# Performance work log

Hardware: AMD Instinct MI355X
Metric: run time of the kernel (lower is better)

Reference implementation:

```python
import jax, jax.numpy as jnp
import numpy as np

DIM = 512
NUM_HEADS = 8
EXPAND = 3
D1 = EXPAND * DIM          # 1536, divisible by NUM_HEADS
HEAD_DIM = D1 // NUM_HEADS  # 192
RPE_DIM = 64
RPE_LAYERS = 3
GLU_DIM = 1024
GAMMA = 0.999
EPS = 1e-8


def srms(x):
    # SimpleRMSNorm: x / (||x||_2 / sqrt(d) + eps), parameter-free
    d = x.shape[-1]
    rms = jnp.linalg.norm(x, axis=-1, keepdims=True) * (d ** -0.5)
    return x / (rms + EPS)


def setup_inputs() -> dict:
    key = jax.random.key(0)
    ks = jax.random.split(key, 12)
    def w(k, shape):
        return jax.random.normal(k, shape, dtype=jnp.float32) * 0.02
    B, H, W = 16, 32, 32
    return {
        "x": jax.random.normal(ks[0], (B, H * W, DIM), dtype=jnp.float32),
        "u_w": w(ks[1], (DIM, D1)), "u_b": jnp.zeros((D1,), jnp.float32),
        "v_w": w(ks[2], (DIM, D1)), "v_b": jnp.zeros((D1,), jnp.float32),
        "o_w": w(ks[3], (D1, DIM)), "o_b": jnp.zeros((DIM,), jnp.float32),
        "pos_w": w(ks[4], (2, RPE_DIM)), "pos_b": jnp.zeros((RPE_DIM,), jnp.float32),
        "rpe_lw": w(ks[5], (RPE_LAYERS, RPE_DIM, RPE_DIM)),
        "rpe_lb": jnp.zeros((RPE_LAYERS, RPE_DIM), jnp.float32),
        "rpe_ow": w(ks[6], (RPE_DIM, NUM_HEADS * HEAD_DIM)),
        "rpe_ob": jnp.zeros((NUM_HEADS * HEAD_DIM,), jnp.float32),
        "l1_w": w(ks[7], (DIM, GLU_DIM)), "l1_b": jnp.zeros((GLU_DIM,), jnp.float32),
        "l2_w": w(ks[8], (DIM, GLU_DIM)), "l2_b": jnp.zeros((GLU_DIM,), jnp.float32),
        "l3_w": w(ks[9], (GLU_DIM, DIM)), "l3_b": jnp.zeros((DIM,), jnp.float32),
        "H": H, "W": W,
    }


def _rpe(pos, pos_w, pos_b, rpe_lw, rpe_lb, rpe_ow, rpe_ob):
    # pos: (P, 2) relative 2D offsets -> (P, NUM_HEADS*HEAD_DIM) Toeplitz coefficients
    x = pos @ pos_w + pos_b
    for i in range(RPE_LAYERS):  # norm -> act -> linear
        x = jax.nn.silu(srms(x)) @ rpe_lw[i] + rpe_lb[i]
    return jax.nn.silu(srms(x)) @ rpe_ow + rpe_ob


def _gtu2d(x, H, W, u_w, u_b, v_w, v_b, o_w, o_b,
           pos_w, pos_b, rpe_lw, rpe_lb, rpe_ow, rpe_ob):
    B, N, _ = x.shape
    u = jax.nn.silu(x @ u_w + u_b)                 # (B, N, D1)
    v = jax.nn.silu(x @ v_w + v_b)                 # (B, N, D1)
    v = v.reshape(B, H, W, NUM_HEADS, HEAD_DIM).transpose(0, 3, 1, 2, 4)  # b h H W d
    # circular layout of relative offsets for FFT lengths (2H, 2W):
    # index a in [0, 2H) maps to offset a if a < H else a - 2H
    di = jnp.concatenate([jnp.arange(H), jnp.arange(-H, 0)]).astype(jnp.float32)
    dj = jnp.concatenate([jnp.arange(W), jnp.arange(-W, 0)]).astype(jnp.float32)
    pos = jnp.stack(jnp.meshgrid(di, dj, indexing="ij"), axis=-1)  # (2H, 2W, 2)
    coef = _rpe(pos.reshape(-1, 2), pos_w, pos_b, rpe_lw, rpe_lb, rpe_ow, rpe_ob)
    coef = coef.reshape(2 * H, 2 * W, NUM_HEADS, HEAD_DIM).transpose(2, 0, 1, 3)  # h 2H 2W d
    # decay mask gamma^(|di|+|dj|)
    decay = GAMMA ** (jnp.abs(di)[:, None] + jnp.abs(dj)[None, :])  # (2H, 2W)
    coef = coef * decay[None, :, :, None]
    # block-Toeplitz token mixing as 2D circular convolution via FFT
    vf = jnp.fft.rfft2(v, s=(2 * H, 2 * W), axes=(2, 3))
    cf = jnp.fft.rfft2(coef, s=(2 * H, 2 * W), axes=(1, 2))
    out = jnp.fft.irfft2(vf * cf[None], s=(2 * H, 2 * W), axes=(2, 3))[:, :, :H, :W, :]
    out = out.transpose(0, 2, 3, 1, 4).reshape(B, N, D1)
    return (u * out) @ o_w + o_b


def reference(x, u_w, u_b, v_w, v_b, o_w, o_b, pos_w, pos_b,
              rpe_lw, rpe_lb, rpe_ow, rpe_ob,
              l1_w, l1_b, l2_w, l2_b, l3_w, l3_b, H, W):
    x = x + _gtu2d(x, H, W, u_w, u_b, v_w, v_b, o_w, o_b,
                   pos_w, pos_b, rpe_lw, rpe_lb, rpe_ow, rpe_ob)
    mlp = (jax.nn.silu(x @ l1_w + l1_b) * (x @ l2_w + l2_b)) @ l3_w + l3_b
    return x + srms(mlp)
```

## Files before the change

kernel.cpp:

```cpp
#include <hip/hip_runtime.h>
#include <math.h>

#define B_   16
#define NN   1024
#define DIM_ 512
#define D1_  1536
#define GLU_ 1024

typedef unsigned short u16;
typedef __attribute__((ext_vector_type(8))) short bf16x8;
typedef __attribute__((ext_vector_type(4))) float f32x4;

__device__ __forceinline__ float silu_f(float x) {
    return x / (1.0f + __expf(-x));
}
__device__ __forceinline__ u16 f2b(float f) {
    unsigned u = __float_as_uint(f);
    return (u16)((u + 0x7FFF + ((u >> 16) & 1)) >> 16);
}
__device__ __forceinline__ float b2f(u16 s) {
    return __uint_as_float(((unsigned)s) << 16);
}

__launch_bounds__(256)
__global__ void prep_kernel(const float* __restrict__ x, u16* __restrict__ xb,
                            const float* __restrict__ u_w, u16* __restrict__ uwT,
                            const float* __restrict__ v_w, u16* __restrict__ vwT,
                            const float* __restrict__ o_w, u16* __restrict__ owT,
                            const float* __restrict__ l1_w, const float* __restrict__ l2_w,
                            u16* __restrict__ gluT,
                            const float* __restrict__ l3_w, u16* __restrict__ l3T,
                            const float* __restrict__ rpe_ow, u16* __restrict__ owT2,
                            const float* __restrict__ l1_b, const float* __restrict__ l2_b,
                            float* __restrict__ gluB,
                            const float* __restrict__ pos_w, const float* __restrict__ pos_b,
                            const float* __restrict__ lw, const float* __restrict__ lb,
                            u16* __restrict__ y) {
    __shared__ __align__(16) char smem_raw[4352];
    int bb = blockIdx.x;
    int t = threadIdx.x;
    if (bb < 2048) {
        #pragma unroll
        for (int j = 0; j < 4; ++j) {
            int i = bb * 1024 + j * 256 + t;
            float4 f = reinterpret_cast<const float4*>(x)[i];
            unsigned lo = (unsigned)f2b(f.x) | ((unsigned)f2b(f.y) << 16);
            unsigned hi = (unsigned)f2b(f.z) | ((unsigned)f2b(f.w) << 16);
            reinterpret_cast<uint2*>(xb)[i] = make_uint2(lo, hi);
        }
    } else if (bb < 5984) {
        const float* in; u16* out; int K, N, tile;
        if (bb < 2816)      { in = u_w;  out = uwT;  K = 512;  N = 1536; tile = bb - 2048; }
        else if (bb < 3584) { in = v_w;  out = vwT;  K = 512;  N = 1536; tile = bb - 2816; }
        else if (bb < 4352) { in = o_w;  out = owT;  K = 1536; N = 512;  tile = bb - 3584; }
        else if (bb < 4864) { in = l1_w; out = gluT; K = 512;  N = 1024; tile = bb - 4352; }
        else if (bb < 5376) { in = l2_w; out = gluT + (size_t)GLU_ * DIM_; K = 512; N = 1024; tile = bb - 4864; }
        else if (bb < 5888) { in = l3_w; out = l3T;  K = 1024; N = 512;  tile = bb - 5376; }
        else                { in = rpe_ow; out = owT2; K = 64; N = 1536; tile = bb - 5888; }
        float (*tl)[33] = (float(*)[33])smem_raw;
        int tiles_x = N >> 5;
        int n0 = (tile % tiles_x) * 32, k0 = (tile / tiles_x) * 32;
        int tx = t & 31, ty = t >> 5;
        #pragma unroll
        for (int r = 0; r < 32; r += 8)
            tl[ty + r][tx] = in[(size_t)(k0 + ty + r) * N + n0 + tx];
        __syncthreads();
        #pragma unroll
        for (int r = 0; r < 32; r += 8)
            out[(size_t)(n0 + ty + r) * K + k0 + tx] = f2b(tl[tx][ty + r]);
    } else if (bb < 5992) {
        int i = (bb - 5984) * 256 + t;
        gluB[i] = (i < 1024) ? l1_b[i] : l2_b[i - 1024];
    } else {
        float (*yb)[64] = (float(*)[64])smem_raw;
        int lane = t & 63;
        int wv = t >> 6;
        int a = (bb - 5992) * 4 + wv;
        int a1 = a >> 6, a2 = a & 63;
        float di = (a1 < 32) ? (float)a1 : (float)(a1 - 64);
        float dj = (a2 < 32) ? (float)a2 : (float)(a2 - 64);
        float xv = di * pos_w[lane] + dj * pos_w[64 + lane] + pos_b[lane];
        for (int L = 0; L < 3; ++L) {
            float ss = xv * xv;
            #pragma unroll
            for (int o = 32; o > 0; o >>= 1) ss += __shfl_xor(ss, o, 64);
            float yv = silu_f(xv / (sqrtf(ss) * 0.125f + 1e-8f));
            yb[wv][lane] = yv;
            __syncthreads();
            float acc = lb[L * 64 + lane];
            const float* w = lw + L * 4096 + lane;
            #pragma unroll 8
            for (int k = 0; k < 64; ++k) acc = fmaf(yb[wv][k], w[k * 64], acc);
            __syncthreads();
            xv = acc;
        }
        float ss = xv * xv;
        #pragma unroll
        for (int o = 32; o > 0; o >>= 1) ss += __shfl_xor(ss, o, 64);
        float yv = silu_f(xv / (sqrtf(ss) * 0.125f + 1e-8f));
        y[(size_t)a * 64 + lane] = f2b(yv);
    }
}

__global__ void coef_tt_kernel(const u16* __restrict__ coefD, u16* __restrict__ coefTT) {
    int t = threadIdx.x;
    int jg = blockIdx.x;
    int ct = blockIdx.y;
    int c  = ct * 64 + (t & 63);
    int jj = t >> 6;
    int dj = jg * 4 + jj;
    float adj = (dj < 32) ? (float)dj : (float)(64 - dj);
    #pragma unroll
    for (int oi = 0; oi < 8; ++oi) {
        u16 vals[8];
        #pragma unroll
        for (int m2 = 0; m2 < 8; ++m2) {
            int di = oi * 8 + m2;
            float adi = (di < 32) ? (float)di : (float)(64 - di);
            float decay = __expf(-0.0010005003335835344f * (adi + adj));
            vals[m2] = f2b(b2f(coefD[(size_t)(di * 64 + dj) * D1_ + c]) * decay);
        }
        *reinterpret_cast<uint4*>(&coefTT[(size_t)c * 4096 + dj * 64 + oi * 8]) =
            *reinterpret_cast<uint4*>(vals);
    }
}

template<int EPI, int PERMB>
__launch_bounds__(256, 4)
__global__ void mfma_gemm(const u16* __restrict__ A, const u16* __restrict__ BT,
                          const float* __restrict__ bias, const float* __restrict__ R,
                          void* __restrict__ C0, void* __restrict__ C1,
                          int M, int N, int K) {
    __shared__ __align__(16) u16 Asmem[128 * 64];
    __shared__ __align__(16) u16 Bsmem[128 * 64];
    int nwg = gridDim.x * gridDim.y;
    int bid = blockIdx.y * gridDim.x + blockIdx.x;
    int qq = nwg >> 3, rr = nwg & 7;
    int xcd = bid & 7, lid = bid >> 3;
    int swz = (xcd < rr ? xcd * (qq + 1) : rr * (qq + 1) + (xcd - rr) * qq) + lid;
    int bx = swz % gridDim.x, by = swz / gridDim.x;
    int tid = threadIdx.x;
    int w = tid >> 6, lane = tid & 63;
    int lr = lane & 15, kg = lane >> 4;
    int wr = w >> 1, wc = w & 1;
    int m0 = by * 128, n0 = bx * 128;
    f32x4 acc[4][4] = {};
    for (int k0 = 0; k0 < K; k0 += 64) {
        #pragma unroll
        for (int r = 0; r < 4; ++r) {
            int c4 = (r * 4 + w) * 64 + lane;
            int row = c4 >> 3, slot = c4 & 7;
            int sl = slot ^ (row & 7);
            const u16* ga = A + (size_t)(m0 + row) * K + k0 + sl * 8;
            int grow = n0 + row;
            if (PERMB == 1) {
                grow = (grow & ~1023) | ((grow & 31) << 5) | ((grow >> 5) & 31);
            } else if (PERMB == 2) {
                int c = grow & 127;
                int f = ((grow >> 7) << 6) + ((c >> 6) << 5) + (((c >> 5) & 1) << 4) + (c & 15);
                grow = (((c >> 4) & 1) << 10) + f;
            }
            const u16* gb = BT + (size_t)grow * K + k0 + sl * 8;
            u16* la = Asmem + (r * 4 + w) * 512;
            u16* lb = Bsmem + (r * 4 + w) * 512;
            __builtin_amdgcn_global_load_lds((const __attribute__((address_space(1))) void*)ga,
                                             (__attribute__((address_space(3))) void*)la, 16, 0, 0);
            __builtin_amdgcn_global_load_lds((const __attribute__((address_space(1))) void*)gb,
                                             (__attribute__((address_space(3))) void*)lb, 16, 0, 0);
        }
        __syncthreads();
        #pragma unroll
        for (int kk = 0; kk < 2; ++kk) {
            bf16x8 af[4], bfr[4];
            #pragma unroll
            for (int m = 0; m < 4; ++m) {
                int row = wr * 64 + m * 16 + lr;
                int sl = (kk * 4 + kg) ^ (row & 7);
                af[m] = *reinterpret_cast<const bf16x8*>(&Asmem[row * 64 + sl * 8]);
            }
            #pragma unroll
            for (int n = 0; n < 4; ++n) {
                int row = wc * 64 + n * 16 + lr;
                int sl = (kk * 4 + kg) ^ (row & 7);
                bfr[n] = *reinterpret_cast<const bf16x8*>(&Bsmem[row * 64 + sl * 8]);
            }
            #pragma unroll
            for (int m = 0; m < 4; ++m)
                #pragma unroll
                for (int n = 0; n < 4; ++n)
                    acc[m][n] = __builtin_amdgcn_mfma_f32_16x16x32_bf16(af[m], bfr[n], acc[m][n], 0, 0, 0);
        }
        __syncthreads();
    }
    if (EPI == 5) {
        #pragma unroll
        for (int m = 0; m < 4; ++m) {
            #pragma unroll
            for (int np = 0; np < 2; ++np) {
                int n = np * 2;
                int f = (n0 >> 1) + wc * 32 + np * 16 + lr;
                #pragma unroll
                for (int q = 0; q < 4; ++q) {
                    int row = m0 + wr * 64 + m * 16 + kg * 4 + q;
                    float a1 = acc[m][n][q] + bias[f];
                    float a2 = acc[m][n + 1][q] + bias[1024 + f];
                    ((u16*)C0)[(size_t)row * GLU_ + f] = f2b(silu_f(a1) * a2);
                }
            }
        }
    } else {
        #pragma unroll
        for (int m = 0; m < 4; ++m) {
            #pragma unroll
            for (int n = 0; n < 4; ++n) {
                #pragma unroll
                for (int q = 0; q < 4; ++q) {
                    int row = m0 + wr * 64 + m * 16 + kg * 4 + q;
                    int col = n0 + wc * 64 + n * 16 + lr;
                    size_t idx = (size_t)row * N + col;
                    if (EPI == 0) {
                        float vv = acc[m][n][q] + bias[col];
                        ((u16*)C0)[idx] = f2b(silu_f(vv));
                    } else if (EPI == 1) {
                        float t2 = acc[m][n][q] + bias[col] + R[idx];
                        ((float*)C0)[idx] = t2;
                        ((u16*)C1)[idx] = f2b(t2);
                    } else if (EPI == 2) {
                        ((u16*)C0)[idx] = f2b(acc[m][n][q] + bias[col]);
                    } else if (EPI == 3) {
                        ((float*)C0)[idx] = acc[m][n][q] + bias[col];
                    } else {
                        float vv = acc[m][n][q] + bias[row];
                        ((u16*)C0)[idx] = f2b(silu_f(vv));
                    }
                }
            }
        }
    }
}

__launch_bounds__(512, 1)
__global__ void conv_mfma_kernel(const u16* __restrict__ coefTT, const u16* __restrict__ vT2,
                                 u16* __restrict__ mixT) {
    __shared__ __align__(16) u16 vlds[16384];
    __shared__ __align__(16) u16 gt[32768];
    __shared__ __align__(16) u16 d2l[4096];
    int c = blockIdx.x;
    int t = threadIdx.x;
    int wv = t >> 6, lane = t & 63;
    int lr = lane & 15, kg = lane >> 4;
    int lrs = lr & 7;

    int mbc[4];
    #pragma unroll
    for (int nt = 0; nt < 4; ++nt)
        mbc[nt] = (((kg * 8 - (nt * 8 + wv)) & 63) & ~7) >> 3;

    #pragma unroll
    for (int pass = 0; pass < 4; ++pass) {
        int L = pass * 512 + t;
        int b = L >> 7, k8s = L & 127;
        int k8 = k8s ^ (b & 7);
        const u16* src = vT2 + (size_t)c * 16384 + b * 1024 + k8 * 8;
        u16* dst = vlds + (size_t)(pass * 512 + wv * 64) * 8;
        __builtin_amdgcn_global_load_lds((const __attribute__((address_space(1))) void*)src,
                                         (__attribute__((address_space(3))) void*)dst, 16, 0, 0);
    }
    {
        const u16* src = coefTT + (size_t)c * 4096 + t * 8;
        u16* dst = d2l + wv * 512;
        __builtin_amdgcn_global_load_lds((const __attribute__((address_space(1))) void*)src,
                                         (__attribute__((address_space(3))) void*)dst, 16, 0, 0);
    }
    __syncthreads();

    for (int e = t; e < 32768; e += 512) {
        int m = e & 63, w = (e >> 6) & 63, o = e >> 12;
        int oo = (8 - o) & 7;
        int q = (64 - ((m + oo) & 63)) & 63;
        gt[(o * 64 + w) * 64 + ((m >> 3) ^ (w & 7)) * 8 + (m & 7)] = d2l[w * 64 + q];
    }
    __syncthreads();

    f32x4 acc[4][2] = {};
    const bf16x8* vb8 = (const bf16x8*)vlds;
    const bf16x8* gtw = (const bf16x8*)gt + wv * 512;
    for (int jp = 0; jp < 32; ++jp) {
        bf16x8 af = vb8[lr * 128 + ((jp * 4 + kg) ^ lrs)];
        int w0 = (lr - jp) & 63;
        int w1 = (w0 + 16) & 63;
        #pragma unroll
        for (int nt = 0; nt < 4; ++nt) {
            bf16x8 b0 = gtw[w0 * 8 + (mbc[nt] ^ (w0 & 7))];
            acc[nt][0] = __builtin_amdgcn_mfma_f32_16x16x32_bf16(af, b0, acc[nt][0], 0, 0, 0);
            bf16x8 b1 = gtw[w1 * 8 + (mbc[nt] ^ (w1 & 7))];
            acc[nt][1] = __builtin_amdgcn_mfma_f32_16x16x32_bf16(af, b1, acc[nt][1], 0, 0, 0);
        }
    }
    __syncthreads();

    #pragma unroll
    for (int nt = 0; nt < 4; ++nt) {
        #pragma unroll
        for (int h = 0; h < 2; ++h) {
            int p = nt * 256 + wv * 32 + h * 16 + lr;
            #pragma unroll
            for (int q = 0; q < 4; ++q) {
                int b = kg * 4 + q;
                vlds[b * 1024 + (p ^ ((b & 7) << 3))] = f2b(acc[nt][h][q]);
            }
        }
    }
    __syncthreads();

    const uint4* src16 = (const uint4*)vlds;
    #pragma unroll
    for (int pass = 0; pass < 4; ++pass) {
        int L = pass * 512 + t;
        int b = L >> 7;
        int pc = (L & 127) ^ (b & 7);
        uint4 val = src16[L];
        *reinterpret_cast<uint4*>(mixT + (size_t)c * 16384 + b * 1024 + pc * 8) = val;
    }
}

__launch_bounds__(256)
__global__ void mult_kernel(const u16* __restrict__ mixT, u16* __restrict__ u) {
    int r = blockIdx.x * 256 + threadIdx.x;
    int c0 = blockIdx.y * 64;
    #pragma unroll
    for (int oc = 0; oc < 8; ++oc) {
        int cb = c0 + oc * 8;
        float mv[8];
        #pragma unroll
        for (int m2 = 0; m2 < 8; ++m2)
            mv[m2] = b2f(mixT[(size_t)(cb + m2) * 16384 + r]);
        u16 uv[8];
        *reinterpret_cast<uint4*>(uv) = *reinterpret_cast<const uint4*>(&u[(size_t)r * D1_ + cb]);
        #pragma unroll
        for (int m2 = 0; m2 < 8; ++m2) uv[m2] = f2b(b2f(uv[m2]) * mv[m2]);
        *reinterpret_cast<uint4*>(&u[(size_t)r * D1_ + cb]) = *reinterpret_cast<uint4*>(uv);
    }
}

__launch_bounds__(256)
__global__ void final_kernel(const float* __restrict__ x2, const float* __restrict__ m,
                             float* __restrict__ out) {
    int row = blockIdx.x;
    const float* mr = m + (size_t)row * DIM_;
    const float* xr = x2 + (size_t)row * DIM_;
    float* orow = out + (size_t)row * DIM_;
    int t = threadIdx.x;
    float a = mr[t], b2 = mr[t + 256];
    float ss = a * a + b2 * b2;
    #pragma unroll
    for (int o = 32; o > 0; o >>= 1) ss += __shfl_xor(ss, o, 64);
    __shared__ float red[4];
    int wid = t >> 6;
    if ((t & 63) == 0) red[wid] = ss;
    __syncthreads();
    float tot = red[0] + red[1] + red[2] + red[3];
    float inv = 1.0f / (sqrtf(tot) * 0.044194173824159216f + 1e-8f);
    orow[t]       = xr[t]       + a  * inv;
    orow[t + 256] = xr[t + 256] + b2 * inv;
}

extern "C" void kernel_launch(void* const* d_in, const int* in_sizes, int n_in,
                              void* d_out, int out_size, void* d_ws, size_t ws_size,
                              hipStream_t stream) {
    const float* x     = (const float*)d_in[0];
    const float* u_w   = (const float*)d_in[1];
    const float* u_b   = (const float*)d_in[2];
    const float* v_w   = (const float*)d_in[3];
    const float* v_b   = (const float*)d_in[4];
    const float* o_w   = (const float*)d_in[5];
    const float* o_b   = (const float*)d_in[6];
    const float* pos_w = (const float*)d_in[7];
    const float* pos_b = (const float*)d_in[8];
    const float* rpe_lw = (const float*)d_in[9];
    const float* rpe_lb = (const float*)d_in[10];
    const float* rpe_ow = (const float*)d_in[11];
    const float* rpe_ob = (const float*)d_in[12];
    const float* l1_w  = (const float*)d_in[13];
    const float* l1_b  = (const float*)d_in[14];
    const float* l2_w  = (const float*)d_in[15];
    const float* l2_b  = (const float*)d_in[16];
    const float* l3_w  = (const float*)d_in[17];
    const float* l3_b  = (const float*)d_in[18];
    float* out = (float*)d_out;

    u16* coefD  = (u16*)d_ws;
    u16* coefTT = coefD + 6291456;
    u16* xb     = coefTT + 6291456;
    u16* u      = xb + 8388608;
    u16* vT2    = u + 25165824;
    u16* mixT   = vT2 + 25165824;
    float* x2   = (float*)(mixT + 25165824);
    u16* x2b    = (u16*)(x2 + 8388608);
    u16* uwT    = x2b + 8388608;
    u16* vwT    = uwT + 786432;
    u16* owT    = vwT + 786432;
    u16* gluT   = owT + 786432;
    u16* l3T    = gluT + 1048576;
    float* gluB = (float*)(l3T + 524288);
    u16* y      = (u16*)(gluB + 2048);
    u16* owT2   = y + 262144;
    u16* p      = u;
    float* mm   = (float*)vT2;

    const int M = B_ * NN;

    prep_kernel<<<7016, 256, 0, stream>>>(x, xb, u_w, uwT, v_w, vwT, o_w, owT,
                                          l1_w, l2_w, gluT, l3_w, l3T, rpe_ow, owT2,
                                          l1_b, l2_b, gluB, pos_w, pos_b, rpe_lw, rpe_lb, y);
    mfma_gemm<2, 0><<<dim3(D1_ / 128, 4096 / 128), 256, 0, stream>>>(y, owT2, rpe_ob, nullptr, coefD, nullptr, 4096, D1_, 64);
    coef_tt_kernel<<<dim3(16, 24), 256, 0, stream>>>(coefD, coefTT);
    mfma_gemm<4, 1><<<dim3(M / 128, D1_ / 128), 256, 0, stream>>>(vwT, xb, v_b, nullptr, vT2, nullptr, D1_, M, DIM_);
    conv_mfma_kernel<<<1536, 512, 0, stream>>>(coefTT, vT2, mixT);
    mfma_gemm<0, 0><<<dim3(D1_ / 128, M / 128), 256, 0, stream>>>(xb, uwT, u_b, nullptr, u, nullptr, M, D1_, DIM_);
    mult_kernel<<<dim3(M / 256, D1_ / 64), 256, 0, stream>>>(mixT, u);
    mfma_gemm<1, 0><<<dim3(DIM_ / 128, M / 128), 256, 0, stream>>>(u, owT, o_b, x, x2, x2b, M, DIM_, D1_);
    mfma_gemm<5, 2><<<dim3(2 * GLU_ / 128, M / 128), 256, 0, stream>>>(x2b, gluT, gluB, nullptr, p, nullptr, M, 2 * GLU_, DIM_);
    mfma_gemm<3, 0><<<dim3(DIM_ / 128, M / 128), 256, 0, stream>>>(p, l3T, l3_b, nullptr, mm, nullptr, M, DIM_, GLU_);
    final_kernel<<<M, 256, 0, stream>>>(x2, mm, out);
}
```

Measured before the change: 396.4 us.

## Fuse decay transpose into coef GEMM epilogue and store residual/MLP in bf16

Removes the separate coef_tt_kernel by computing the coefficient GEMM transposed (weights as A, permuted positions as B) and applying the decay factor in a new epilogue, writing coefTT directly. It also drops the fp32 copies of the residual x2 and the l3 output, keeping only bf16 versions that final_kernel reads. This cuts a launch and a sizeable amount of fp32 memory traffic. The cost is precision: the residual stream added into the output is now rounded to bf16.

```diff
diff --git a/kernel.cpp b/kernel.cpp
--- a/kernel.cpp
+++ b/kernel.cpp
@@ -99,29 +99,6 @@
         for (int o = 32; o > 0; o >>= 1) ss += __shfl_xor(ss, o, 64);
         float yv = silu_f(xv / (sqrtf(ss) * 0.125f + 1e-8f));
         y[(size_t)a * 64 + lane] = f2b(yv);
-    }
-}
-
-__global__ void coef_tt_kernel(const u16* __restrict__ coefD, u16* __restrict__ coefTT) {
-    int t = threadIdx.x;
-    int jg = blockIdx.x;
-    int ct = blockIdx.y;
-    int c  = ct * 64 + (t & 63);
-    int jj = t >> 6;
-    int dj = jg * 4 + jj;
-    float adj = (dj < 32) ? (float)dj : (float)(64 - dj);
-    #pragma unroll
-    for (int oi = 0; oi < 8; ++oi) {
-        u16 vals[8];
-        #pragma unroll
-        for (int m2 = 0; m2 < 8; ++m2) {
-            int di = oi * 8 + m2;
-            float adi = (di < 32) ? (float)di : (float)(64 - di);
-            float decay = __expf(-0.0010005003335835344f * (adi + adj));
-            vals[m2] = f2b(b2f(coefD[(size_t)(di * 64 + dj) * D1_ + c]) * decay);
-        }
-        *reinterpret_cast<uint4*>(&coefTT[(size_t)c * 4096 + dj * 64 + oi * 8]) =
-            *reinterpret_cast<uint4*>(vals);
     }
 }
 
@@ -159,6 +136,8 @@
                 int c = grow & 127;
                 int f = ((grow >> 7) << 6) + ((c >> 6) << 5) + (((c >> 5) & 1) << 4) + (c & 15);
                 grow = (((c >> 4) & 1) << 10) + f;
+            } else if (PERMB == 3) {
+                grow = ((grow & 63) << 6) | ((grow >> 6) & 63);
             }
             const u16* gb = BT + (size_t)grow * K + k0 + sl * 8;
             u16* la = Asmem + (r * 4 + w) * 512;
@@ -222,16 +201,18 @@
                         float vv = acc[m][n][q] + bias[col];
                         ((u16*)C0)[idx] = f2b(silu_f(vv));
                     } else if (EPI == 1) {
-                        float t2 = acc[m][n][q] + bias[col] + R[idx];
-                        ((float*)C0)[idx] = t2;
-                        ((u16*)C1)[idx] = f2b(t2);
+                        ((u16*)C0)[idx] = f2b(acc[m][n][q] + bias[col] + R[idx]);
                     } else if (EPI == 2) {
                         ((u16*)C0)[idx] = f2b(acc[m][n][q] + bias[col]);
-                    } else if (EPI == 3) {
-                        ((float*)C0)[idx] = acc[m][n][q] + bias[col];
-                    } else {
+                    } else if (EPI == 4) {
                         float vv = acc[m][n][q] + bias[row];
                         ((u16*)C0)[idx] = f2b(silu_f(vv));
+                    } else {
+                        int dii = col & 63, djj = (col >> 6) & 63;
+                        float adi = (dii < 32) ? (float)dii : (float)(64 - dii);
+                        float adj = (djj < 32) ? (float)djj : (float)(64 - djj);
+                        float decay = __expf(-0.0010005003335835344f * (adi + adj));
+                        ((u16*)C0)[idx] = f2b((acc[m][n][q] + bias[row]) * decay);
                     }
                 }
             }
@@ -344,14 +325,14 @@
 }
 
 __launch_bounds__(256)
-__global__ void final_kernel(const float* __restrict__ x2, const float* __restrict__ m,
+__global__ void final_kernel(const u16* __restrict__ x2b, const u16* __restrict__ m,
                              float* __restrict__ out) {
     int row = blockIdx.x;
-    const float* mr = m + (size_t)row * DIM_;
-    const float* xr = x2 + (size_t)row * DIM_;
+    const u16* mr = m + (size_t)row * DIM_;
+    const u16* xr = x2b + (size_t)row * DIM_;
     float* orow = out + (size_t)row * DIM_;
     int t = threadIdx.x;
-    float a = mr[t], b2 = mr[t + 256];
+    float a = b2f(mr[t]), b2 = b2f(mr[t + 256]);
     float ss = a * a + b2 * b2;
     #pragma unroll
     for (int o = 32; o > 0; o >>= 1) ss += __shfl_xor(ss, o, 64);
@@ -361,8 +342,8 @@
     __syncthreads();
     float tot = red[0] + red[1] + red[2] + red[3];
     float inv = 1.0f / (sqrtf(tot) * 0.044194173824159216f + 1e-8f);
-    orow[t]       = xr[t]       + a  * inv;
-    orow[t + 256] = xr[t + 256] + b2 * inv;
+    orow[t]       = b2f(xr[t])       + a  * inv;
+    orow[t + 256] = b2f(xr[t + 256]) + b2 * inv;
 }
 
 extern "C" void kernel_launch(void* const* d_in, const int* in_sizes, int n_in,
@@ -389,14 +370,12 @@
     const float* l3_b  = (const float*)d_in[18];
     float* out = (float*)d_out;
 
-    u16* coefD  = (u16*)d_ws;
-    u16* coefTT = coefD + 6291456;
+    u16* coefTT = (u16*)d_ws;
     u16* xb     = coefTT + 6291456;
     u16* u      = xb + 8388608;
     u16* vT2    = u + 25165824;
     u16* mixT   = vT2 + 25165824;
-    float* x2   = (float*)(mixT + 25165824);
-    u16* x2b    = (u16*)(x2 + 8388608);
+    u16* x2b    = mixT + 25165824;
     u16* uwT    = x2b + 8388608;
     u16* vwT    = uwT + 786432;
     u16* owT    = vwT + 786432;
@@ -406,21 +385,20 @@
     u16* y      = (u16*)(gluB + 2048);
     u16* owT2   = y + 262144;
     u16* p      = u;
-    float* mm   = (float*)vT2;
+    u16* mm     = vT2;
 
     const int M = B_ * NN;
 
     prep_kernel<<<7016, 256, 0, stream>>>(x, xb, u_w, uwT, v_w, vwT, o_w, owT,
                                           l1_w, l2_w, gluT, l3_w, l3T, rpe_ow, owT2,
                                           l1_b, l2_b, gluB, pos_w, pos_b, rpe_lw, rpe_lb, y);
-    mfma_gemm<2, 0><<<dim3(D1_ / 128, 4096 / 128), 256, 0, stream>>>(y, owT2, rpe_ob, nullptr, coefD, nullptr, 4096, D1_, 64);
-    coef_tt_kernel<<<dim3(16, 24), 256, 0, stream>>>(coefD, coefTT);
+    mfma_gemm<6, 3><<<dim3(4096 / 128, D1_ / 128), 256, 0, stream>>>(owT2, y, rpe_ob, nullptr, coefTT, nullptr, D1_, 4096, 64);
     mfma_gemm<4, 1><<<dim3(M / 128, D1_ / 128), 256, 0, stream>>>(vwT, xb, v_b, nullptr, vT2, nullptr, D1_, M, DIM_);
     conv_mfma_kernel<<<1536, 512, 0, stream>>>(coefTT, vT2, mixT);
     mfma_gemm<0, 0><<<dim3(D1_ / 128, M / 128), 256, 0, stream>>>(xb, uwT, u_b, nullptr, u, nullptr, M, D1_, DIM_);
     mult_kernel<<<dim3(M / 256, D1_ / 64), 256, 0, stream>>>(mixT, u);
-    mfma_gemm<1, 0><<<dim3(DIM_ / 128, M / 128), 256, 0, stream>>>(u, owT, o_b, x, x2, x2b, M, DIM_, D1_);
+    mfma_gemm<1, 0><<<dim3(DIM_ / 128, M / 128), 256, 0, stream>>>(u, owT, o_b, x, x2b, nullptr, M, DIM_, D1_);
     mfma_gemm<5, 2><<<dim3(2 * GLU_ / 128, M / 128), 256, 0, stream>>>(x2b, gluT, gluB, nullptr, p, nullptr, M, 2 * GLU_, DIM_);
-    mfma_gemm<3, 0><<<dim3(DIM_ / 128, M / 128), 256, 0, stream>>>(p, l3T, l3_b, nullptr, mm, nullptr, M, DIM_, GLU_);
-    final_kernel<<<M, 256, 0, stream>>>(x2, mm, out);
-}
+    mfma_gemm<2, 0><<<dim3(DIM_ / 128, M / 128), 256, 0, stream>>>(p, l3T, l3_b, nullptr, mm, nullptr, M, DIM_, GLU_);
+    final_kernel<<<M, 256, 0, stream>>>(x2b, mm, out);
+}
```

After: 369.0 us. 1.07x faster.
